# Performance work log

Hardware: AMD Instinct MI355X
Metric: run time of the kernel (lower is better)

Reference implementation:

```python
import jax, jax.numpy as jnp
import numpy as np

N_NODES = 10000
N_EDGES = 640000
NFEAT = 128
NHID = 128
NCLASS = 40
DROP = 0.5


def setup_inputs() -> dict:
    key = jax.random.key(0)
    ks = jax.random.split(key, 12)
    inp = {
        "x": jax.random.normal(ks[0], (N_NODES, NFEAT), dtype=jnp.float32),
        "edge_index": jax.random.randint(ks[1], (2, N_EDGES), 0, N_NODES, dtype=jnp.int64),
        "W0": jax.random.normal(ks[2], (NHID, NFEAT), dtype=jnp.float32) * (1.0 / np.sqrt(NFEAT)),
        "b0": jax.random.normal(ks[3], (NHID,), dtype=jnp.float32) * 0.01,
        "W1": jax.random.normal(ks[4], (NHID, NHID), dtype=jnp.float32) * (1.0 / np.sqrt(NHID)),
        "b1": jax.random.normal(ks[5], (NHID,), dtype=jnp.float32) * 0.01,
        "W2": jax.random.normal(ks[6], (NHID, NHID), dtype=jnp.float32) * (1.0 / np.sqrt(NHID)),
        "b2": jax.random.normal(ks[7], (NHID,), dtype=jnp.float32) * 0.01,
        "p_drop": jnp.full((NHID,), DROP, dtype=jnp.float32),
        "Wl": jax.random.normal(ks[8], (NCLASS, NHID), dtype=jnp.float32) * (1.0 / np.sqrt(NHID)),
        "bl": jax.random.normal(ks[9], (NCLASS,), dtype=jnp.float32) * 0.01,
    }
    return inp


def reference(x, edge_index, W0, b0, W1, b1, W2, b2, p_drop, Wl, bl):
    src = edge_index[0]
    dst = edge_index[1]
    # deterministic variational dropout mask (shared across layers)
    mask = jnp.clip(p_drop, 0.0, 1.0)[None, :]  # [1, nhid]
    h = x
    for W, b in ((W0, b0), (W1, b1), (W2, b2)):
        # GINConv, eps=0: h_i' = Linear(h_i + sum_{j->i} h_j)
        agg = jax.ops.segment_sum(h[src], dst, num_segments=N_NODES)  # [N, d]
        h = (h + agg) @ W.T + b
        h = jax.nn.relu(h) * mask
    return h @ Wl.T + bl
```

## Files before the change

kernel.cpp:

```cpp
#include <hip/hip_runtime.h>

#define NN 10000
#define NE 640000
#define D 128
#define NC 40
#define CAP 128
#define NBKT 313
#define BCAP 2304
#define NBIN 157
#define DEPTH 24

typedef unsigned short u16;
typedef unsigned int u32;
typedef short bf16x8 __attribute__((ext_vector_type(8)));
typedef float f32x4v __attribute__((ext_vector_type(4)));

__device__ __forceinline__ float bf2f(u16 u) { return __uint_as_float(((u32)u) << 16); }
__device__ __forceinline__ u16 f2bf(float f) {
    u32 u = __float_as_uint(f);
    u += 0x7fff + ((u >> 16) & 1);
    return (u16)(u >> 16);
}
__device__ __forceinline__ void upadd(u32 w, float& a, float& b) {
    a += __uint_as_float(w << 16);
    b += __uint_as_float(w & 0xffff0000u);
}

__global__ __launch_bounds__(256) void zero_kernel(uint4* __restrict__ p, int n4) {
    int i = blockIdx.x * 256 + threadIdx.x;
    if (i < n4) p[i] = make_uint4(0u, 0u, 0u, 0u);
}

__global__ __launch_bounds__(256) void phaseA(const float* __restrict__ x,
        const int* __restrict__ src, const int* __restrict__ dst,
        const float* __restrict__ W0, const float* __restrict__ W1, const float* __restrict__ W2,
        int* __restrict__ gcur, u32* __restrict__ gbucket,
        u16* __restrict__ whi, u16* __restrict__ wlo, u16* __restrict__ G) {
    __shared__ union {
        struct { u32 bin[NBKT][DEPTH]; int bcnt[NBKT]; int gbase[NBKT]; u32 ovf[128][2]; int ocnt; } a;
        u16 Gs[32 * 128];
    } sm;
    int b = blockIdx.x, t = threadIdx.x;
    if (b < NBIN) {
        for (int i = t; i < NBKT; i += 256) sm.a.bcnt[i] = 0;
        if (t == 0) sm.a.ocnt = 0;
        __syncthreads();
        #pragma unroll
        for (int rep = 0; rep < 4; rep++) {
            int e0 = b * 4096 + rep * 1024 + t * 4;
            if (e0 < NE) {
                int4 d4 = *reinterpret_cast<const int4*>(dst + e0);
                int4 s4 = *reinterpret_cast<const int4*>(src + e0);
                int dd[4] = {d4.x, d4.y, d4.z, d4.w};
                int ss[4] = {s4.x, s4.y, s4.z, s4.w};
                #pragma unroll
                for (int i = 0; i < 4; i++) {
                    int bk = dd[i] >> 5;
                    u32 entry = ((u32)(dd[i] & 31) << 16) | (u32)ss[i];
                    int pos = atomicAdd(&sm.a.bcnt[bk], 1);
                    if (pos < DEPTH) sm.a.bin[bk][pos] = entry;
                    else {
                        int o = atomicAdd(&sm.a.ocnt, 1);
                        if (o < 128) { sm.a.ovf[o][0] = ((u32)bk << 16) | (u32)pos; sm.a.ovf[o][1] = entry; }
                    }
                }
            }
        }
        __syncthreads();
        for (int i = t; i < NBKT; i += 256) {
            int n = sm.a.bcnt[i];
            sm.a.gbase[i] = n ? atomicAdd(&gcur[i * 16], n) : 0;
        }
        __syncthreads();
        for (int idx = t; idx < NBKT * DEPTH; idx += 256) {
            int bk = idx / DEPTH, j = idx - bk * DEPTH;
            int n = sm.a.bcnt[bk];
            if (j < (n > DEPTH ? DEPTH : n)) {
                int p = sm.a.gbase[bk] + j;
                if (p < BCAP) gbucket[(size_t)bk * BCAP + p] = sm.a.bin[bk][j];
            }
        }
        int oc = sm.a.ocnt; if (oc > 128) oc = 128;
        for (int i = t; i < oc; i += 256) {
            int bk = (int)(sm.a.ovf[i][0] >> 16);
            int pos = (int)(sm.a.ovf[i][0] & 0xffff);
            int p = sm.a.gbase[bk] + pos;
            if (p >= 0 && p < BCAP) gbucket[(size_t)bk * BCAP + p] = sm.a.ovf[i][1];
        }
    } else if (b < NBIN + 313) {
        int nb0 = (b - NBIN) * 32;
        int wid = t >> 6, l = t & 63;
        int m = l & 15, gq = l >> 4;
        int mt = wid & 1, nh = wid >> 1;
        int nodeA = nb0 + mt * 16 + m;
        if (nodeA >= NN) nodeA = NN - 1;
        const float* xr = x + (size_t)nodeA * 128;
        f32x4v acc[4];
        #pragma unroll
        for (int nt = 0; nt < 4; nt++) acc[nt] = (f32x4v){0.f, 0.f, 0.f, 0.f};
        #pragma unroll
        for (int ks = 0; ks < 4; ks++) {
            float4 a0 = *reinterpret_cast<const float4*>(xr + ks * 32 + gq * 8);
            float4 a1 = *reinterpret_cast<const float4*>(xr + ks * 32 + gq * 8 + 4);
            float av[8] = {a0.x, a0.y, a0.z, a0.w, a1.x, a1.y, a1.z, a1.w};
            union { uint4 u; bf16x8 v; } ca;
            u32 ap[4];
            #pragma unroll
            for (int j = 0; j < 4; j++)
                ap[j] = (u32)f2bf(av[2 * j]) | ((u32)f2bf(av[2 * j + 1]) << 16);
            ca.u = make_uint4(ap[0], ap[1], ap[2], ap[3]);
            #pragma unroll
            for (int nt = 0; nt < 4; nt++) {
                int n = nh * 64 + nt * 16 + m;
                const float* wr = W0 + (size_t)n * 128 + ks * 32 + gq * 8;
                float4 w0 = *reinterpret_cast<const float4*>(wr);
                float4 w1 = *reinterpret_cast<const float4*>(wr + 4);
                float wv[8] = {w0.x, w0.y, w0.z, w0.w, w1.x, w1.y, w1.z, w1.w};
                u32 hp[4], lp[4];
                #pragma unroll
                for (int j = 0; j < 4; j++) {
                    u16 h0 = f2bf(wv[2 * j]), h1 = f2bf(wv[2 * j + 1]);
                    float r0 = wv[2 * j] - bf2f(h0), r1 = wv[2 * j + 1] - bf2f(h1);
                    hp[j] = (u32)h0 | ((u32)h1 << 16);
                    lp[j] = (u32)f2bf(r0) | ((u32)f2bf(r1) << 16);
                }
                union { uint4 u; bf16x8 v; } ch, cl;
                ch.u = make_uint4(hp[0], hp[1], hp[2], hp[3]);
                cl.u = make_uint4(lp[0], lp[1], lp[2], lp[3]);
                acc[nt] = __builtin_amdgcn_mfma_f32_16x16x32_bf16(ca.v, ch.v, acc[nt], 0, 0, 0);
                acc[nt] = __builtin_amdgcn_mfma_f32_16x16x32_bf16(ca.v, cl.v, acc[nt], 0, 0, 0);
            }
        }
        #pragma unroll
        for (int nt = 0; nt < 4; nt++) {
            #pragma unroll
            for (int j = 0; j < 4; j++) {
                int mm = mt * 16 + gq * 4 + j;
                int n = nh * 64 + nt * 16 + m;
                sm.Gs[mm * 128 + (n ^ ((mm & 7) << 4))] = f2bf(acc[nt][j]);
            }
        }
        __syncthreads();
        #pragma unroll
        for (int i = 0; i < 2; i++) {
            int c = t + i * 256;
            int mm = c >> 4, n0 = (c & 15) * 8;
            int node = nb0 + mm;
            if (node < NN) {
                uint4 v = *reinterpret_cast<const uint4*>(&sm.Gs[mm * 128 + (n0 ^ ((mm & 7) << 4))]);
                *reinterpret_cast<uint4*>(G + (size_t)node * 128 + n0) = v;
            }
        }
    } else {
        int idx = (b - (NBIN + 313)) * 2048 + t * 8;
        int wi = idx >> 14, off = idx & 16383;
        const float* W = wi ? W2 : W1;
        float4 v0 = *reinterpret_cast<const float4*>(W + off);
        float4 v1 = *reinterpret_cast<const float4*>(W + off + 4);
        float wv[8] = {v0.x, v0.y, v0.z, v0.w, v1.x, v1.y, v1.z, v1.w};
        u16 ho[8], lo[8];
        #pragma unroll
        for (int j = 0; j < 8; j++) {
            u16 h = f2bf(wv[j]);
            ho[j] = h;
            lo[j] = f2bf(wv[j] - bf2f(h));
        }
        *reinterpret_cast<uint4*>(whi + idx + 16384) = *reinterpret_cast<uint4*>(ho);
        *reinterpret_cast<uint4*>(wlo + idx + 16384) = *reinterpret_cast<uint4*>(lo);
    }
}

__global__ __launch_bounds__(256) void phaseB(const int* __restrict__ gcur,
        const u32* __restrict__ gbucket, u16* __restrict__ csr, int* __restrict__ cnt) {
    __shared__ u16 slice[32 * CAP];
    __shared__ int scnt[32];
    int b = blockIdx.x, t = threadIdx.x;
    if (t < 32) scnt[t] = 0;
    __syncthreads();
    int total = gcur[b * 16];
    if (total > BCAP) total = BCAP;
    for (int i = t; i < total; i += 256) {
        u32 e = gbucket[(size_t)b * BCAP + i];
        int dl = (int)((e >> 16) & 31);
        int pos = atomicAdd(&scnt[dl], 1);
        if (pos < CAP) slice[dl * CAP + pos] = (u16)(e & 0xffff);
    }
    __syncthreads();
    int node0 = b * 32;
    const u32* s32 = reinterpret_cast<const u32*>(slice);
    u32* c32 = reinterpret_cast<u32*>(csr) + (size_t)node0 * 64;
    for (int i = t; i < 2048; i += 256) {
        if (node0 + (i >> 6) < NN) c32[i] = s32[i];
    }
    if (t < 32) {
        int node = node0 + t;
        if (node < NN) cnt[node] = scnt[t] > CAP ? CAP : scnt[t];
    }
}

template<bool LAST>
__global__ __launch_bounds__(1024) void fuse_kernel(
        const u16* __restrict__ gin, const int* __restrict__ cnt, const u16* __restrict__ csr,
        const float* __restrict__ bias, const float* __restrict__ pd,
        const u16* __restrict__ wh, const u16* __restrict__ wl_, u16* __restrict__ gout,
        const float* __restrict__ Wl, const float* __restrict__ bl, float* __restrict__ out) {
    __shared__ u16 nbr[16][128];
    __shared__ union {
        u16 A[16 * 128];
        struct { float WlS[NC * 129]; float rows[16 * D]; float blS[NC]; } c;
    } sm;
    const int t = threadIdx.x, wid = t >> 6, ln = t & 63;
    const int q = ln >> 4, fq = ln & 15, fo8 = fq << 3;
    const int nb0 = blockIdx.x * 16;
    const int node = nb0 + wid;

    if (LAST) {
        for (int i = t; i < NC * D; i += 1024) sm.c.WlS[(i >> 7) * 129 + (i & 127)] = Wl[i];
        if (t < NC) sm.c.blS[t] = bl[t];
    }

    int c_ = cnt[node];
    if (c_ > CAP) c_ = CAP;
    *reinterpret_cast<u32*>(&nbr[wid][ln << 1]) =
        *reinterpret_cast<const u32*>(csr + ((size_t)node << 7) + (ln << 1));

    float va[8] = {0.f, 0.f, 0.f, 0.f, 0.f, 0.f, 0.f, 0.f};
    if (q == 0) {
        uint4 v = *reinterpret_cast<const uint4*>(gin + ((size_t)node << 7) + fo8);
        upadd(v.x, va[0], va[1]); upadd(v.y, va[2], va[3]);
        upadd(v.z, va[4], va[5]); upadd(v.w, va[6], va[7]);
    }
    int iters = (c_ + 31) >> 5;
    for (int i = 0; i < iters; i++) {
        int b0 = (i << 5) + (q << 2);
        int b1 = b0 + 16;
        ushort4 ia = *reinterpret_cast<const ushort4*>(&nbr[wid][b0]);
        ushort4 ib = *reinterpret_cast<const ushort4*>(&nbr[wid][b1]);
        int id0 = (b0 + 0 < c_) ? (int)ia.x : node;
        int id1 = (b0 + 1 < c_) ? (int)ia.y : node;
        int id2 = (b0 + 2 < c_) ? (int)ia.z : node;
        int id3 = (b0 + 3 < c_) ? (int)ia.w : node;
        int id4 = (b1 + 0 < c_) ? (int)ib.x : node;
        int id5 = (b1 + 1 < c_) ? (int)ib.y : node;
        int id6 = (b1 + 2 < c_) ? (int)ib.z : node;
        int id7 = (b1 + 3 < c_) ? (int)ib.w : node;
        uint4 v0 = *reinterpret_cast<const uint4*>(gin + ((size_t)id0 << 7) + fo8);
        uint4 v1 = *reinterpret_cast<const uint4*>(gin + ((size_t)id1 << 7) + fo8);
        uint4 v2 = *reinterpret_cast<const uint4*>(gin + ((size_t)id2 << 7) + fo8);
        uint4 v3 = *reinterpret_cast<const uint4*>(gin + ((size_t)id3 << 7) + fo8);
        uint4 v4 = *reinterpret_cast<const uint4*>(gin + ((size_t)id4 << 7) + fo8);
        uint4 v5 = *reinterpret_cast<const uint4*>(gin + ((size_t)id5 << 7) + fo8);
        uint4 v6 = *reinterpret_cast<const uint4*>(gin + ((size_t)id6 << 7) + fo8);
        uint4 v7 = *reinterpret_cast<const uint4*>(gin + ((size_t)id7 << 7) + fo8);
        if (b0 + 0 < c_) { upadd(v0.x, va[0], va[1]); upadd(v0.y, va[2], va[3]); upadd(v0.z, va[4], va[5]); upadd(v0.w, va[6], va[7]); }
        if (b0 + 1 < c_) { upadd(v1.x, va[0], va[1]); upadd(v1.y, va[2], va[3]); upadd(v1.z, va[4], va[5]); upadd(v1.w, va[6], va[7]); }
        if (b0 + 2 < c_) { upadd(v2.x, va[0], va[1]); upadd(v2.y, va[2], va[3]); upadd(v2.z, va[4], va[5]); upadd(v2.w, va[6], va[7]); }
        if (b0 + 3 < c_) { upadd(v3.x, va[0], va[1]); upadd(v3.y, va[2], va[3]); upadd(v3.z, va[4], va[5]); upadd(v3.w, va[6], va[7]); }
        if (b1 + 0 < c_) { upadd(v4.x, va[0], va[1]); upadd(v4.y, va[2], va[3]); upadd(v4.z, va[4], va[5]); upadd(v4.w, va[6], va[7]); }
        if (b1 + 1 < c_) { upadd(v5.x, va[0], va[1]); upadd(v5.y, va[2], va[3]); upadd(v5.z, va[4], va[5]); upadd(v5.w, va[6], va[7]); }
        if (b1 + 2 < c_) { upadd(v6.x, va[0], va[1]); upadd(v6.y, va[2], va[3]); upadd(v6.z, va[4], va[5]); upadd(v6.w, va[6], va[7]); }
        if (b1 + 3 < c_) { upadd(v7.x, va[0], va[1]); upadd(v7.y, va[2], va[3]); upadd(v7.z, va[4], va[5]); upadd(v7.w, va[6], va[7]); }
    }
    #pragma unroll
    for (int j = 0; j < 8; j++) {
        va[j] += __shfl_xor(va[j], 16);
        va[j] += __shfl_xor(va[j], 32);
    }
    if (ln < 16) {
        float4 bv0 = *reinterpret_cast<const float4*>(bias + fo8);
        float4 bv1 = *reinterpret_cast<const float4*>(bias + fo8 + 4);
        float4 mv0 = *reinterpret_cast<const float4*>(pd + fo8);
        float4 mv1 = *reinterpret_cast<const float4*>(pd + fo8 + 4);
        float bb[8] = {bv0.x, bv0.y, bv0.z, bv0.w, bv1.x, bv1.y, bv1.z, bv1.w};
        float mm[8] = {mv0.x, mv0.y, mv0.z, mv0.w, mv1.x, mv1.y, mv1.z, mv1.w};
        float r[8];
        #pragma unroll
        for (int j = 0; j < 8; j++) {
            float mk = fminf(fmaxf(mm[j], 0.f), 1.f);
            r[j] = fmaxf(va[j] + bb[j], 0.f) * mk;
        }
        if (LAST) {
            #pragma unroll
            for (int j = 0; j < 8; j++) sm.c.rows[wid * D + fo8 + j] = r[j];
        } else {
            u32 p0 = (u32)f2bf(r[0]) | ((u32)f2bf(r[1]) << 16);
            u32 p1 = (u32)f2bf(r[2]) | ((u32)f2bf(r[3]) << 16);
            u32 p2 = (u32)f2bf(r[4]) | ((u32)f2bf(r[5]) << 16);
            u32 p3 = (u32)f2bf(r[6]) | ((u32)f2bf(r[7]) << 16);
            *reinterpret_cast<uint4*>(&sm.A[wid * 128 + ((fq ^ (wid & 7)) << 3)]) =
                make_uint4(p0, p1, p2, p3);
        }
    }
    __syncthreads();

    if (LAST) {
        if (t < 16 * NC) {
            int n = t / NC, c = t - n * NC;
            const float* rr = &sm.c.rows[n * D];
            const float* wr = &sm.c.WlS[c * 129];
            float acc = sm.c.blS[c];
            #pragma unroll 8
            for (int k = 0; k < D; k++) acc = fmaf(rr[k], wr[k], acc);
            out[(size_t)(nb0 + n) * NC + c] = acc;
        }
        return;
    }

    int m = ln & 15, gq = ln >> 4;
    bf16x8 afr[4];
    if (wid < 8) {
        #pragma unroll
        for (int ks = 0; ks < 4; ks++) {
            int chunk = gq + ks * 4;
            afr[ks] = *reinterpret_cast<const bf16x8*>(&sm.A[m * 128 + ((chunk ^ (m & 7)) << 3)]);
        }
    }
    __syncthreads();
    if (wid < 8) {
        f32x4v acc = (f32x4v){0.f, 0.f, 0.f, 0.f};
        int n = wid * 16 + m;
        const u16* whp = wh + (size_t)n * 128;
        const u16* wlp = wl_ + (size_t)n * 128;
        #pragma unroll
        for (int ks = 0; ks < 4; ks++) {
            bf16x8 bh = *reinterpret_cast<const bf16x8*>(whp + ks * 32 + gq * 8);
            bf16x8 bl = *reinterpret_cast<const bf16x8*>(wlp + ks * 32 + gq * 8);
            acc = __builtin_amdgcn_mfma_f32_16x16x32_bf16(afr[ks], bh, acc, 0, 0, 0);
            acc = __builtin_amdgcn_mfma_f32_16x16x32_bf16(afr[ks], bl, acc, 0, 0, 0);
        }
        u16* Gs = sm.A;
        #pragma unroll
        for (int j = 0; j < 4; j++) {
            int mm = gq * 4 + j;
            Gs[mm * 128 + (n ^ ((mm & 7) << 4))] = f2bf(acc[j]);
        }
    }
    __syncthreads();
    if (t < 256) {
        const u16* Gs = sm.A;
        int mm = t >> 4, n0 = (t & 15) * 8;
        uint4 v = *reinterpret_cast<const uint4*>(&Gs[mm * 128 + (n0 ^ ((mm & 7) << 4))]);
        *reinterpret_cast<uint4*>(gout + (size_t)(nb0 + mm) * 128 + n0) = v;
    }
}

extern "C" void kernel_launch(void* const* d_in, const int* in_sizes, int n_in,
                              void* d_out, int out_size, void* d_ws, size_t ws_size,
                              hipStream_t stream) {
    const float* x  = (const float*)d_in[0];
    const int*   ei = (const int*)d_in[1];
    const float* W0 = (const float*)d_in[2];
    const float* b0 = (const float*)d_in[3];
    const float* W1 = (const float*)d_in[4];
    const float* b1 = (const float*)d_in[5];
    const float* W2 = (const float*)d_in[6];
    const float* b2 = (const float*)d_in[7];
    const float* pd = (const float*)d_in[8];
    const float* Wl = (const float*)d_in[9];
    const float* bl = (const float*)d_in[10];

    char* ws = (char*)d_ws;
    int* gcur    = (int*)ws;
    int* cnt     = (int*)(ws + 20480);
    u16* csr     = (u16*)(ws + 61440);
    u16* gbA     = (u16*)(ws + 2621440);
    u16* gbB     = (u16*)(ws + 5181440);
    u32* gbucket = (u32*)(ws + 5181440);
    u16* whi     = (u16*)(ws + 8066048);
    u16* wlo     = (u16*)(ws + 8164352);

    const int* src = ei;
    const int* dst = ei + NE;

    zero_kernel<<<5, 256, 0, stream>>>((uint4*)gcur, 1280);
    phaseA<<<NBIN + 313 + 16, 256, 0, stream>>>(x, src, dst, W0, W1, W2, gcur, gbucket, whi, wlo, gbA);
    phaseB<<<NBKT, 256, 0, stream>>>(gcur, gbucket, csr, cnt);
    fuse_kernel<false><<<625, 1024, 0, stream>>>(gbA, cnt, csr, b0, pd,
                                                 whi + 16384, wlo + 16384, gbB,
                                                 nullptr, nullptr, nullptr);
    fuse_kernel<false><<<625, 1024, 0, stream>>>(gbB, cnt, csr, b1, pd,
                                                 whi + 32768, wlo + 32768, gbA,
                                                 nullptr, nullptr, nullptr);
    fuse_kernel<true><<<625, 1024, 0, stream>>>(gbA, cnt, csr, b2, pd,
                                                nullptr, nullptr, nullptr,
                                                Wl, bl, (float*)d_out);
}
```

Measured before the change: 99.13 us.

## Replace global atomic bucket offsets with fixed per-block slots and overflow lists

```diff
diff --git a/kernel.cpp b/kernel.cpp
--- a/kernel.cpp
+++ b/kernel.cpp
@@ -6,9 +6,9 @@
 #define NC 40
 #define CAP 128
 #define NBKT 313
-#define BCAP 2304
 #define NBIN 157
 #define DEPTH 24
+#define OVFB 64
 
 typedef unsigned short u16;
 typedef unsigned int u32;
@@ -26,18 +26,14 @@
     b += __uint_as_float(w & 0xffff0000u);
 }
 
-__global__ __launch_bounds__(256) void zero_kernel(uint4* __restrict__ p, int n4) {
-    int i = blockIdx.x * 256 + threadIdx.x;
-    if (i < n4) p[i] = make_uint4(0u, 0u, 0u, 0u);
-}
-
 __global__ __launch_bounds__(256) void phaseA(const float* __restrict__ x,
         const int* __restrict__ src, const int* __restrict__ dst,
         const float* __restrict__ W0, const float* __restrict__ W1, const float* __restrict__ W2,
-        int* __restrict__ gcur, u32* __restrict__ gbucket,
+        u32* __restrict__ gbucket, int* __restrict__ bcnt_g,
+        int* __restrict__ ovfcnt, u32* __restrict__ ovf2,
         u16* __restrict__ whi, u16* __restrict__ wlo, u16* __restrict__ G) {
     __shared__ union {
-        struct { u32 bin[NBKT][DEPTH]; int bcnt[NBKT]; int gbase[NBKT]; u32 ovf[128][2]; int ocnt; } a;
+        struct { u32 bin[NBKT][DEPTH]; int bcnt[NBKT]; u32 ovfl[OVFB]; int ocnt; } a;
         u16 Gs[32 * 128];
     } sm;
     int b = blockIdx.x, t = threadIdx.x;
@@ -55,38 +51,30 @@
                 int ss[4] = {s4.x, s4.y, s4.z, s4.w};
                 #pragma unroll
                 for (int i = 0; i < 4; i++) {
-                    int bk = dd[i] >> 5;
-                    u32 entry = ((u32)(dd[i] & 31) << 16) | (u32)ss[i];
+                    int bk = dd[i] >> 5, dl = dd[i] & 31;
+                    u32 entry = ((u32)dl << 16) | (u32)ss[i];
                     int pos = atomicAdd(&sm.a.bcnt[bk], 1);
                     if (pos < DEPTH) sm.a.bin[bk][pos] = entry;
                     else {
                         int o = atomicAdd(&sm.a.ocnt, 1);
-                        if (o < 128) { sm.a.ovf[o][0] = ((u32)bk << 16) | (u32)pos; sm.a.ovf[o][1] = entry; }
+                        if (o < OVFB) sm.a.ovfl[o] = ((u32)bk << 21) | ((u32)dl << 16) | (u32)ss[i];
                     }
                 }
             }
-        }
-        __syncthreads();
-        for (int i = t; i < NBKT; i += 256) {
-            int n = sm.a.bcnt[i];
-            sm.a.gbase[i] = n ? atomicAdd(&gcur[i * 16], n) : 0;
         }
         __syncthreads();
         for (int idx = t; idx < NBKT * DEPTH; idx += 256) {
             int bk = idx / DEPTH, j = idx - bk * DEPTH;
-            int n = sm.a.bcnt[bk];
-            if (j < (n > DEPTH ? DEPTH : n)) {
-                int p = sm.a.gbase[bk] + j;
-                if (p < BCAP) gbucket[(size_t)bk * BCAP + p] = sm.a.bin[bk][j];
-            }
-        }
-        int oc = sm.a.ocnt; if (oc > 128) oc = 128;
-        for (int i = t; i < oc; i += 256) {
-            int bk = (int)(sm.a.ovf[i][0] >> 16);
-            int pos = (int)(sm.a.ovf[i][0] & 0xffff);
-            int p = sm.a.gbase[bk] + pos;
-            if (p >= 0 && p < BCAP) gbucket[(size_t)bk * BCAP + p] = sm.a.ovf[i][1];
-        }
+            int n = sm.a.bcnt[bk]; if (n > DEPTH) n = DEPTH;
+            if (j < n) gbucket[(size_t)bk * (NBIN * DEPTH) + b * DEPTH + j] = sm.a.bin[bk][j];
+        }
+        for (int i = t; i < NBKT; i += 256) {
+            int n = sm.a.bcnt[i];
+            bcnt_g[i * NBIN + b] = n > DEPTH ? DEPTH : n;
+        }
+        int oc = sm.a.ocnt; if (oc > OVFB) oc = OVFB;
+        if (t == 0) ovfcnt[b] = oc;
+        for (int i = t; i < oc; i += 256) ovf2[b * OVFB + i] = sm.a.ovfl[i];
     } else if (b < NBIN + 313) {
         int nb0 = (b - NBIN) * 32;
         int wid = t >> 6, l = t & 63;
@@ -170,23 +158,42 @@
     }
 }
 
-__global__ __launch_bounds__(256) void phaseB(const int* __restrict__ gcur,
-        const u32* __restrict__ gbucket, u16* __restrict__ csr, int* __restrict__ cnt) {
+__global__ __launch_bounds__(256) void phaseB(const u32* __restrict__ gbucket,
+        const int* __restrict__ bcnt_g, const int* __restrict__ ovfcnt, const u32* __restrict__ ovf2,
+        u16* __restrict__ csr, int* __restrict__ cnt) {
     __shared__ u16 slice[32 * CAP];
     __shared__ int scnt[32];
-    int b = blockIdx.x, t = threadIdx.x;
+    __shared__ int lcnt[NBIN];
+    __shared__ int locnt[NBIN];
+    int bk = blockIdx.x, t = threadIdx.x;
     if (t < 32) scnt[t] = 0;
-    __syncthreads();
-    int total = gcur[b * 16];
-    if (total > BCAP) total = BCAP;
-    for (int i = t; i < total; i += 256) {
-        u32 e = gbucket[(size_t)b * BCAP + i];
-        int dl = (int)((e >> 16) & 31);
-        int pos = atomicAdd(&scnt[dl], 1);
-        if (pos < CAP) slice[dl * CAP + pos] = (u16)(e & 0xffff);
-    }
-    __syncthreads();
-    int node0 = b * 32;
+    for (int i = t; i < NBIN; i += 256) { lcnt[i] = bcnt_g[bk * NBIN + i]; locnt[i] = ovfcnt[i]; }
+    __syncthreads();
+    const u32* gb = gbucket + (size_t)bk * (NBIN * DEPTH);
+    for (int idx = t; idx < NBIN * DEPTH; idx += 256) {
+        int b = idx / DEPTH, j = idx - b * DEPTH;
+        if (j < lcnt[b]) {
+            u32 e = gb[idx];
+            int dl = (int)((e >> 16) & 31);
+            int pos = atomicAdd(&scnt[dl], 1);
+            if (pos < CAP) slice[dl * CAP + pos] = (u16)(e & 0xffff);
+        }
+    }
+    for (int b = 0; b < NBIN; b++) {
+        int n = locnt[b];
+        if (n > 0) {
+            for (int i = t; i < n; i += 256) {
+                u32 e = ovf2[b * OVFB + i];
+                if ((int)(e >> 21) == bk) {
+                    int dl = (int)((e >> 16) & 31);
+                    int pos = atomicAdd(&scnt[dl], 1);
+                    if (pos < CAP) slice[dl * CAP + pos] = (u16)(e & 0xffff);
+                }
+            }
+        }
+    }
+    __syncthreads();
+    int node0 = bk * 32;
     const u32* s32 = reinterpret_cast<const u32*>(slice);
     u32* c32 = reinterpret_cast<u32*>(csr) + (size_t)node0 * 64;
     for (int i = t; i < 2048; i += 256) {
@@ -360,21 +367,23 @@
     const float* bl = (const float*)d_in[10];
 
     char* ws = (char*)d_ws;
-    int* gcur    = (int*)ws;
-    int* cnt     = (int*)(ws + 20480);
-    u16* csr     = (u16*)(ws + 61440);
-    u16* gbA     = (u16*)(ws + 2621440);
-    u16* gbB     = (u16*)(ws + 5181440);
-    u32* gbucket = (u32*)(ws + 5181440);
-    u16* whi     = (u16*)(ws + 8066048);
-    u16* wlo     = (u16*)(ws + 8164352);
+    int* cnt     = (int*)ws;
+    u16* csr     = (u16*)(ws + 40960);
+    u16* gbA     = (u16*)(ws + 2600960);
+    u32* gbucket = (u32*)(ws + 5160960);
+    u16* gbB     = (u16*)(ws + 5160960);
+    int* bcnt_g  = (int*)(ws + 9878496);
+    int* ovfcnt  = (int*)(ws + 10075072);
+    u32* ovf2    = (u32*)(ws + 10075712);
+    u16* whi     = (u16*)(ws + 10115904);
+    u16* wlo     = (u16*)(ws + 10214208);
 
     const int* src = ei;
     const int* dst = ei + NE;
 
-    zero_kernel<<<5, 256, 0, stream>>>((uint4*)gcur, 1280);
-    phaseA<<<NBIN + 313 + 16, 256, 0, stream>>>(x, src, dst, W0, W1, W2, gcur, gbucket, whi, wlo, gbA);
-    phaseB<<<NBKT, 256, 0, stream>>>(gcur, gbucket, csr, cnt);
+    phaseA<<<NBIN + 313 + 16, 256, 0, stream>>>(x, src, dst, W0, W1, W2,
+                                                gbucket, bcnt_g, ovfcnt, ovf2, whi, wlo, gbA);
+    phaseB<<<NBKT, 256, 0, stream>>>(gbucket, bcnt_g, ovfcnt, ovf2, csr, cnt);
     fuse_kernel<false><<<625, 1024, 0, stream>>>(gbA, cnt, csr, b0, pd,
                                                  whi + 16384, wlo + 16384, gbB,
                                                  nullptr, nullptr, nullptr);
```

New measurement: 125.4 us. 1.26x slower.
